# Kernel optimization log

Hardware: AMD Instinct MI355X
Metric: run time of the kernel (lower is better)

Reference implementation:

```python
import jax, jax.numpy as jnp
import numpy as np

TAU = 0.07
EPS = 1e-12  # torch F.normalize eps


def _conv2d(x, w, b, stride):
    # x: (N, Cin, H, W), w: (Cout, Cin, kh, kw)
    y = jax.lax.conv_general_dilated(
        x, w, window_strides=(stride, stride), padding='SAME',
        dimension_numbers=('NCHW', 'OIHW', 'NCHW'))
    return y + b[None, :, None, None]


def _encoder(x, conv1_w, conv1_b, conv2_w, conv2_b, lin_w, lin_b):
    # x: (BTN, 1, H, W) -> (BTN, emb_dim)
    h = jax.nn.relu(_conv2d(x, conv1_w, conv1_b, 2))   # (BTN, 32, H/2, W/2)
    h = jax.nn.relu(_conv2d(h, conv2_w, conv2_b, 2))   # (BTN, 64, H/4, W/4)
    h = h.mean(axis=(2, 3))                            # global avg pool -> (BTN, 64)
    return h @ lin_w + lin_b                           # (BTN, emb_dim)


def setup_inputs() -> dict:
    key = jax.random.key(0)
    ks = jax.random.split(key, 4)
    B, T, N, H, W = 8, 10, 128, 32, 32
    seq = jax.random.normal(ks[0], (B, T, N, H, W), dtype=jnp.float32)
    conv1_w = jax.random.normal(ks[1], (32, 1, 3, 3), dtype=jnp.float32) * (1.0 / 3.0)
    conv1_b = jnp.zeros((32,), jnp.float32)
    conv2_w = jax.random.normal(ks[2], (64, 32, 3, 3), dtype=jnp.float32) * (1.0 / np.sqrt(32 * 9))
    conv2_b = jnp.zeros((64,), jnp.float32)
    lin_w = jax.random.normal(ks[3], (64, 128), dtype=jnp.float32) * (1.0 / 8.0)
    lin_b = jnp.zeros((128,), jnp.float32)
    return {"seq": seq, "conv1_w": conv1_w, "conv1_b": conv1_b,
            "conv2_w": conv2_w, "conv2_b": conv2_b, "lin_w": lin_w, "lin_b": lin_b}


def reference(seq, conv1_w, conv1_b, conv2_w, conv2_b, lin_w, lin_b):
    B, T, N, H, W = seq.shape
    x = seq.reshape(-1, 1, H, W)
    emb = _encoder(x, conv1_w, conv1_b, conv2_w, conv2_b, lin_w, lin_b)
    emb = emb.reshape(B, T, N, -1)
    # L2 normalize along feature dim (torch F.normalize semantics)
    nrm = jnp.sqrt(jnp.sum(emb * emb, axis=-1, keepdims=True))
    emb = emb / jnp.maximum(nrm, EPS)
    # pairwise affinities between consecutive frames: (B, T-1, N, N)
    A = jnp.einsum('btnc,btmc->btnm', emb[:, :-1], emb[:, 1:]) / TAU
    # forward + time-reversed (transposed) affinities: (B, 2(T-1), N, N)
    AA = jnp.concatenate([A, jnp.swapaxes(jnp.flip(A, axis=1), -1, -2)], axis=1)
    S = jax.nn.softmax(AA, axis=-1)  # row-stochastic transition matrices
    I = jnp.eye(N, dtype=seq.dtype)
    loss = jnp.zeros((), seq.dtype)
    for k in range(1, T - 1):
        S_this = jnp.concatenate([S[:, :k], S[:, -k:]], axis=1)  # (B, 2k, N, N)
        At = jnp.broadcast_to(I, (B, N, N))
        for t in range(1, 2 * k):  # note: index 0 unused, matching original
            At = jnp.matmul(S_this[:, t], At)
        # cross_entropy(input=At (B,C=N,d=N), target=eye) with soft targets:
        # mean over (B, d) of -log_softmax(At, class_dim=1)[b, j, j]
        logp = jax.nn.log_softmax(At, axis=1)
        loss = loss - jnp.mean(jnp.diagonal(logp, axis1=1, axis2=2))
    return (loss / N, A)
```

## Files before the change

kernel.cpp:

```cpp
#include <hip/hip_runtime.h>
#include <math.h>

typedef _Float16 f16;
typedef f16 f16x8 __attribute__((ext_vector_type(8)));
typedef f16 f16x4 __attribute__((ext_vector_type(4)));
typedef float f32x4 __attribute__((ext_vector_type(4)));

__global__ __launch_bounds__(256) void k_repack(const float* __restrict__ w2,
                                                const float* __restrict__ w1,
                                                const float* __restrict__ lw,
                                                f16* __restrict__ w2p,
                                                f16* __restrict__ w1p,
                                                float* __restrict__ lwT,
                                                float* __restrict__ lossAcc) {
  const int i = blockIdx.x * 256 + threadIdx.x;
  if (i == 0) lossAcc[0] = 0.f;
  if (i < 18432) {
    const int ic = i & 31, oc = (i >> 5) & 63, tap = i >> 11;
    const float w = w2[oc * 288 + ic * 9 + tap];
    const f16 wh = (f16)w;
    w2p[i] = wh;
    w2p[18432 + i] = (f16)(w - (float)wh);
  }
  if (i < 1024) {
    const int oc = i >> 5, k = i & 31;
    f16 r = (f16)0.f;
    if (k < 9) r = (f16)w1[oc * 9 + k];
    else if (k >= 16 && k < 25) {
      const float w = w1[oc * 9 + (k - 16)];
      r = (f16)(w - (float)((f16)w));
    }
    w1p[i] = r;
  }
  if (i < 8192) lwT[i] = lw[(i & 63) * 128 + (i >> 6)];
}

__global__ __launch_bounds__(256, 4) void k_encoder(
    const float* __restrict__ seq,
    const f16* __restrict__ w1p, const float* __restrict__ b1,
    const f16* __restrict__ w2p, const float* __restrict__ b2,
    const float* __restrict__ lwT, const float* __restrict__ lb,
    f16* __restrict__ emb16)
{
  __shared__ float s_in[33 * 33];
  __shared__ __align__(16) f16 s_h1[289 * 40];
  __shared__ __align__(16) float s_pool[64];
  __shared__ float s_part[2];
  const int t = threadIdx.x, lane = t & 63, wv = t >> 6;
  const int lr = lane & 15, lg = lane >> 4;

  const float* x = seq + (size_t)blockIdx.x * 1024;
  for (int i = t; i < 1024; i += 256)
    s_in[(i >> 5) * 33 + (i & 31)] = x[i];
  if (t < 33) s_in[32 * 33 + t] = 0.f;
  if (t < 32) s_in[t * 33 + 32] = 0.f;
  if (t < 132) {
    const int zi = t >> 2, ch = t & 3;
    const int row = (zi < 16) ? zi * 17 + 16 : 272 + (zi - 16);
    *(f32x4*)&s_h1[row * 40 + ch * 8] = f32x4{0.f, 0.f, 0.f, 0.f};
  }
  f16x8 w1f[2];
  float b1v[2];
#pragma unroll
  for (int n = 0; n < 2; ++n) {
    w1f[n] = *(const f16x8*)(w1p + (n * 16 + lr) * 32 + lg * 8);
    b1v[n] = b1[n * 16 + lr];
  }
  __syncthreads();

  {
    const bool odd = lg & 1;
    f32x4 a1[4][2];
#pragma unroll
    for (int m = 0; m < 4; ++m) {
      const int oy = wv * 4 + m;
      const int base = 66 * oy + 2 * lr;
      f16x8 af;
      af[0] = (f16)s_in[base + (odd ? 68 : 0)];
      { const float v = s_in[base + 1];  af[1] = odd ? (f16)0.f : (f16)v; }
      { const float v = s_in[base + 2];  af[2] = odd ? (f16)0.f : (f16)v; }
      { const float v = s_in[base + 33]; af[3] = odd ? (f16)0.f : (f16)v; }
      { const float v = s_in[base + 34]; af[4] = odd ? (f16)0.f : (f16)v; }
      { const float v = s_in[base + 35]; af[5] = odd ? (f16)0.f : (f16)v; }
      { const float v = s_in[base + 66]; af[6] = odd ? (f16)0.f : (f16)v; }
      { const float v = s_in[base + 67]; af[7] = odd ? (f16)0.f : (f16)v; }
#pragma unroll
      for (int n = 0; n < 2; ++n) {
        const f32x4 c0 = f32x4{b1v[n], b1v[n], b1v[n], b1v[n]};
        a1[m][n] = __builtin_amdgcn_mfma_f32_16x16x32_f16(af, w1f[n], c0, 0, 0, 0);
      }
    }
#pragma unroll
    for (int m = 0; m < 4; ++m) {
      const int oy = wv * 4 + m;
#pragma unroll
      for (int n = 0; n < 2; ++n)
#pragma unroll
        for (int v = 0; v < 4; ++v)
          s_h1[(oy * 17 + lg * 4 + v) * 40 + n * 16 + lr] = (f16)fmaxf(a1[m][n][v], 0.f);
    }
  }
  f16x8 bh[9], bl[9];
  float bias2;
  {
    const int oc = wv * 16 + lr;
#pragma unroll
    for (int tap = 0; tap < 9; ++tap) {
      bh[tap] = *(const f16x8*)(w2p + ((tap * 64 + oc) * 32 + lg * 8));
      bl[tap] = *(const f16x8*)(w2p + 18432 + ((tap * 64 + oc) * 32 + lg * 8));
    }
    bias2 = b2[oc];
  }
  __syncthreads();

  {
    f32x4 acc[4];
#pragma unroll
    for (int m = 0; m < 4; ++m) acc[m] = f32x4{bias2, bias2, bias2, bias2};
#pragma unroll
    for (int m = 0; m < 4; ++m) {
      const int opos = m * 16 + lr, oy = opos >> 3, ox = opos & 7;
      const int baddr = (34 * oy + 2 * ox) * 40 + lg * 8;
#pragma unroll
      for (int dy = 0; dy < 3; ++dy)
#pragma unroll
        for (int dx = 0; dx < 3; ++dx) {
          const int tap = dy * 3 + dx;
          const f16x8 afr = *(const f16x8*)&s_h1[baddr + (dy * 17 + dx) * 40];
          acc[m] = __builtin_amdgcn_mfma_f32_16x16x32_f16(afr, bh[tap], acc[m], 0, 0, 0);
          acc[m] = __builtin_amdgcn_mfma_f32_16x16x32_f16(afr, bl[tap], acc[m], 0, 0, 0);
        }
    }
    float s = 0.f;
#pragma unroll
    for (int m = 0; m < 4; ++m)
#pragma unroll
      for (int v = 0; v < 4; ++v) s += fmaxf(acc[m][v], 0.f);
    s += __shfl_xor(s, 16, 64);
    s += __shfl_xor(s, 32, 64);
    if (lane < 16) s_pool[wv * 16 + lane] = s * (1.f / 64.f);
  }
  __syncthreads();
  float val = 0.f;
  if (t < 128) {
    val = lb[t];
    const float* lrow = lwT + t * 64;
#pragma unroll
    for (int c4 = 0; c4 < 16; ++c4) {
      const f32x4 wv4 = *(const f32x4*)(lrow + c4 * 4);
      const f32x4 pv = *(const f32x4*)&s_pool[c4 * 4];
      val = fmaf(pv[0], wv4[0], val);
      val = fmaf(pv[1], wv4[1], val);
      val = fmaf(pv[2], wv4[2], val);
      val = fmaf(pv[3], wv4[3], val);
    }
  }
  float sq = val * val;
#pragma unroll
  for (int off = 1; off < 64; off <<= 1) sq += __shfl_xor(sq, off, 64);
  if (t < 128 && (t & 63) == 0) s_part[t >> 6] = sq;
  __syncthreads();
  if (t < 128) {
    const float nrm = sqrtf(s_part[0] + s_part[1]);
    emb16[(size_t)blockIdx.x * 128 + t] = (f16)(val / fmaxf(nrm, 1e-12f));
  }
}

__global__ __launch_bounds__(256) void k_affsm(
    const f16* __restrict__ emb16, float* __restrict__ Aout,
    f16* __restrict__ Srow, f16* __restrict__ ST, float* __restrict__ loss)
{
  __shared__ __align__(16) f16 sL[16384];
  __shared__ __align__(16) f16 sR[16384];
  __shared__ __align__(16) f16 sT[128 * 136];
  __shared__ float s_cm[128], s_cd[128];
  __shared__ float s_red4[512];
  __shared__ float s_lred[4];
  const int bid = blockIdx.x, b = bid / 9, tt = bid % 9;
  const int t = threadIdx.x, lane = t & 63, w = t >> 6;
  const int lr = lane & 15, lg = lane >> 4;
  const f16* Ea = emb16 + (size_t)(b * 10 + tt) * 16384;
  const f16* Eb = Ea + 16384;
#pragma unroll
  for (int j = 0; j < 8; ++j) {
    const int ck = j * 256 + t, row = ck >> 4, c16 = ck & 15;
    const int off = ((row << 8) + (c16 << 4)) ^ ((row & 7) << 4);
    *(f16x8*)((char*)sL + off) = *(const f16x8*)(Ea + ck * 8);
    *(f16x8*)((char*)sR + off) = *(const f16x8*)(Eb + ck * 8);
  }
  __syncthreads();
  f32x4 acc[2][8] = {};
#pragma unroll
  for (int kt = 0; kt < 4; ++kt) {
    int row = w * 32 + lr;
    int byt = ((row << 8) + kt * 64 + (lg << 4)) ^ ((row & 7) << 4);
    const f16x8 a0 = *(const f16x8*)((char*)sL + byt);
    row += 16;
    byt = ((row << 8) + kt * 64 + (lg << 4)) ^ ((row & 7) << 4);
    const f16x8 a1 = *(const f16x8*)((char*)sL + byt);
#pragma unroll
    for (int nt = 0; nt < 8; ++nt) {
      const int rb = nt * 16 + lr;
      const int bb = ((rb << 8) + kt * 64 + (lg << 4)) ^ ((rb & 7) << 4);
      const f16x8 bv = *(const f16x8*)((char*)sR + bb);
      acc[0][nt] = __builtin_amdgcn_mfma_f32_16x16x32_f16(a0, bv, acc[0][nt], 0, 0, 0);
      acc[1][nt] = __builtin_amdgcn_mfma_f32_16x16x32_f16(a1, bv, acc[1][nt], 0, 0, 0);
    }
  }
#pragma unroll
  for (int mt = 0; mt < 2; ++mt)
#pragma unroll
    for (int nt = 0; nt < 8; ++nt)
#pragma unroll
      for (int v = 0; v < 4; ++v) acc[mt][nt][v] *= (1.f / 0.07f);

  float* Og = Aout + (size_t)bid * 16384;
#pragma unroll
  for (int mt = 0; mt < 2; ++mt)
#pragma unroll
    for (int nt = 0; nt < 8; ++nt)
#pragma unroll
      for (int v = 0; v < 4; ++v)
        Og[(w * 32 + mt * 16 + lg * 4 + v) * 128 + nt * 16 + lr] = acc[mt][nt][v];

  float rm[2][4], rd[2][4];
#pragma unroll
  for (int mt = 0; mt < 2; ++mt)
#pragma unroll
    for (int v = 0; v < 4; ++v) {
      float m = -1e30f;
#pragma unroll
      for (int nt = 0; nt < 8; ++nt) m = fmaxf(m, acc[mt][nt][v]);
      m = fmaxf(m, __shfl_xor(m, 1, 64));
      m = fmaxf(m, __shfl_xor(m, 2, 64));
      m = fmaxf(m, __shfl_xor(m, 4, 64));
      m = fmaxf(m, __shfl_xor(m, 8, 64));
      float s = 0.f;
#pragma unroll
      for (int nt = 0; nt < 8; ++nt) s += expf(acc[mt][nt][v] - m);
      s += __shfl_xor(s, 1, 64);
      s += __shfl_xor(s, 2, 64);
      s += __shfl_xor(s, 4, 64);
      s += __shfl_xor(s, 8, 64);
      rm[mt][v] = m;
      rd[mt][v] = 1.f / s;
    }
#pragma unroll
  for (int nt = 0; nt < 8; ++nt) {
    float m = -1e30f;
#pragma unroll
    for (int mt = 0; mt < 2; ++mt)
#pragma unroll
      for (int v = 0; v < 4; ++v) m = fmaxf(m, acc[mt][nt][v]);
    m = fmaxf(m, __shfl_xor(m, 16, 64));
    m = fmaxf(m, __shfl_xor(m, 32, 64));
    if (lg == 0) s_red4[(nt * 16 + lr) * 4 + w] = m;
  }
  __syncthreads();
  if (t < 128) s_cm[t] = fmaxf(fmaxf(s_red4[t * 4], s_red4[t * 4 + 1]),
                               fmaxf(s_red4[t * 4 + 2], s_red4[t * 4 + 3]));
  __syncthreads();
#pragma unroll
  for (int nt = 0; nt < 8; ++nt) {
    const float mc = s_cm[nt * 16 + lr];
    float s = 0.f;
#pragma unroll
    for (int mt = 0; mt < 2; ++mt)
#pragma unroll
      for (int v = 0; v < 4; ++v) s += expf(acc[mt][nt][v] - mc);
    s += __shfl_xor(s, 16, 64);
    s += __shfl_xor(s, 32, 64);
    if (lg == 0) s_red4[(nt * 16 + lr) * 4 + w] = s;
  }
  __syncthreads();
  if (t < 128) s_cd[t] = 1.f / (s_red4[t * 4] + s_red4[t * 4 + 1] +
                                s_red4[t * 4 + 2] + s_red4[t * 4 + 3]);
  __syncthreads();

  const bool wantSfD = (tt >= 2 && tt <= 7);
  const bool wantSfT = (tt == 1);
  const bool wantSbD = (tt >= 1 && tt <= 7);
  const bool wantSbT = (tt == 0);
  f16* SfD = Srow + (size_t)(b * 18 + tt) * 16384;
  f16* SbD = ST + (size_t)(b * 18 + 17 - tt) * 16384;

  float contrib = 0.f;
#pragma unroll
  for (int mt = 0; mt < 2; ++mt)
#pragma unroll
    for (int v = 0; v < 4; ++v) {
      const int r = w * 32 + mt * 16 + lg * 4 + v;
      float qsum = 0.f, dval = 0.f;
#pragma unroll
      for (int nt = 0; nt < 8; ++nt) {
        const int c = nt * 16 + lr;
        const float a = acc[mt][nt][v];
        const float sf = expf(a - rm[mt][v]) * rd[mt][v];
        const float sb = expf(a - s_cm[c]) * s_cd[c];
        if (wantSfD) SfD[r * 128 + c] = (f16)sf;
        if (wantSbD) SbD[r * 128 + c] = (f16)sb;
        if (wantSfT) sT[c * 136 + r] = (f16)sf;
        if (wantSbT) {
          sT[c * 136 + r] = (f16)sb;
          qsum += expf(sb);
          if (nt == (w * 2 + mt)) dval = sb;
        }
      }
      if (wantSbT) {
        qsum += __shfl_xor(qsum, 1, 64);
        qsum += __shfl_xor(qsum, 2, 64);
        qsum += __shfl_xor(qsum, 4, 64);
        qsum += __shfl_xor(qsum, 8, 64);
        if (lr == lg * 4 + v) contrib += dval - logf(qsum);
      }
    }
  if (wantSfT || wantSbT) {
    __syncthreads();
    f16* dst = wantSfT ? (ST + (size_t)(b * 18 + 1) * 16384)
                       : (Srow + (size_t)(b * 18 + 17) * 16384);
#pragma unroll
    for (int j = 0; j < 8; ++j) {
      const int e = (j * 256 + t) * 8;
      *(f16x8*)(dst + e) = *(const f16x8*)&sT[(e >> 7) * 136 + (e & 127)];
    }
  }
  if (wantSbT) {
#pragma unroll
    for (int off = 1; off < 64; off <<= 1) contrib += __shfl_xor(contrib, off, 64);
    if (lane == 0) s_lred[w] = contrib;
    __syncthreads();
    if (t == 0) atomicAdd(loss, s_lred[0] + s_lred[1] + s_lred[2] + s_lred[3]);
  }
}

__global__ __launch_bounds__(256) void k_chain(
    int k,
    const f16* __restrict__ Srow, const f16* __restrict__ ST,
    f16* __restrict__ Pcur, const f16* __restrict__ Pprev,
    f16* __restrict__ FTcur, const f16* __restrict__ FTprev,
    float* __restrict__ loss)
{
  __shared__ __align__(16) f16 sL[16384];
  __shared__ __align__(16) f16 sRt[16384];
  const int role = blockIdx.x >> 3, b = blockIdx.x & 7;
  const int t = threadIdx.x, lane = t & 63, w = t >> 6;
  const int lr = lane & 15, lg = lane >> 4;

  const f16 *L, *Rt;
  if (role == 0) {
    if (k > 8) return;
    L = (k == 2) ? (Srow + (size_t)(b * 18 + 17) * 16384) : (Pprev + (size_t)b * 16384);
    Rt = ST + (size_t)(b * 18 + (18 - k)) * 16384;
  } else if (role == 1) {
    if (k < 3 || k > 8) return;
    L = Srow + (size_t)(b * 18 + (k - 1)) * 16384;
    Rt = (k == 3) ? (ST + (size_t)(b * 18 + 1) * 16384) : (FTprev + (size_t)b * 16384);
  } else {
    if (k < 3) return;
    L = Pprev + (size_t)b * 16384;
    Rt = (k == 3) ? (ST + (size_t)(b * 18 + 1) * 16384) : (FTprev + (size_t)b * 16384);
  }
#pragma unroll
  for (int j = 0; j < 8; ++j) {
    const int ck = j * 256 + t, row = ck >> 4, c16 = ck & 15;
    const int off = ((row << 8) + (c16 << 4)) ^ ((row & 7) << 4);
    *(f16x8*)((char*)sL + off) = *(const f16x8*)(L + ck * 8);
    *(f16x8*)((char*)sRt + off) = *(const f16x8*)(Rt + ck * 8);
  }
  __syncthreads();
  f32x4 acc[2][8] = {};
#pragma unroll
  for (int kt = 0; kt < 4; ++kt) {
    int row = w * 32 + lr;
    int byt = ((row << 8) + kt * 64 + (lg << 4)) ^ ((row & 7) << 4);
    const f16x8 a0 = *(const f16x8*)((char*)sL + byt);
    row += 16;
    byt = ((row << 8) + kt * 64 + (lg << 4)) ^ ((row & 7) << 4);
    const f16x8 a1 = *(const f16x8*)((char*)sL + byt);
#pragma unroll
    for (int nt = 0; nt < 8; ++nt) {
      const int rb = nt * 16 + lr;
      const int bb = ((rb << 8) + kt * 64 + (lg << 4)) ^ ((rb & 7) << 4);
      const f16x8 bv = *(const f16x8*)((char*)sRt + bb);
      acc[0][nt] = __builtin_amdgcn_mfma_f32_16x16x32_f16(a0, bv, acc[0][nt], 0, 0, 0);
      acc[1][nt] = __builtin_amdgcn_mfma_f32_16x16x32_f16(a1, bv, acc[1][nt], 0, 0, 0);
    }
  }
  if (role == 0) {
    f16* P = Pcur + (size_t)b * 16384;
#pragma unroll
    for (int mt = 0; mt < 2; ++mt)
#pragma unroll
      for (int nt = 0; nt < 8; ++nt)
#pragma unroll
        for (int v = 0; v < 4; ++v)
          P[(w * 32 + mt * 16 + lg * 4 + v) * 128 + nt * 16 + lr] = (f16)acc[mt][nt][v];
  } else if (role == 1) {
    f16* FT = FTcur + (size_t)b * 16384;
#pragma unroll
    for (int mt = 0; mt < 2; ++mt)
#pragma unroll
      for (int nt = 0; nt < 8; ++nt) {
        f16x4 pk;
#pragma unroll
        for (int v = 0; v < 4; ++v) pk[v] = (f16)acc[mt][nt][v];
        *(f16x4*)(FT + (size_t)(nt * 16 + lr) * 128 + w * 32 + mt * 16 + lg * 4) = pk;
      }
  } else {
    __syncthreads();
    float* redm = (float*)sL;
    float* redM = redm + 512;
    float* reds = redM + 128;
    float* redL = reds + 512;
    float* redW = redL + 128;
#pragma unroll
    for (int nt = 0; nt < 8; ++nt) {
      float pm = -1e30f;
#pragma unroll
      for (int mt = 0; mt < 2; ++mt)
#pragma unroll
        for (int v = 0; v < 4; ++v) pm = fmaxf(pm, acc[mt][nt][v]);
      pm = fmaxf(pm, __shfl_xor(pm, 16, 64));
      pm = fmaxf(pm, __shfl_xor(pm, 32, 64));
      if (lg == 0) redm[(nt * 16 + lr) * 4 + w] = pm;
    }
    __syncthreads();
    if (t < 128) redM[t] = fmaxf(fmaxf(redm[t * 4], redm[t * 4 + 1]),
                                 fmaxf(redm[t * 4 + 2], redm[t * 4 + 3]));
    __syncthreads();
#pragma unroll
    for (int nt = 0; nt < 8; ++nt) {
      const float mc = redM[nt * 16 + lr];
      float ps = 0.f;
#pragma unroll
      for (int mt = 0; mt < 2; ++mt)
#pragma unroll
        for (int v = 0; v < 4; ++v) ps += expf(acc[mt][nt][v] - mc);
      ps += __shfl_xor(ps, 16, 64);
      ps += __shfl_xor(ps, 32, 64);
      if (lg == 0) reds[(nt * 16 + lr) * 4 + w] = ps;
    }
    __syncthreads();
    if (t < 128) redL[t] = logf(reds[t * 4] + reds[t * 4 + 1] +
                                reds[t * 4 + 2] + reds[t * 4 + 3]);
    __syncthreads();
    float contrib = 0.f;
#pragma unroll
    for (int mt = 0; mt < 2; ++mt)
#pragma unroll
      for (int nt = 0; nt < 8; ++nt)
#pragma unroll
        for (int v = 0; v < 4; ++v) {
          const int r = w * 32 + mt * 16 + lg * 4 + v, c = nt * 16 + lr;
          if (r == c) contrib += acc[mt][nt][v] - redM[c] - redL[c];
        }
#pragma unroll
    for (int off = 1; off < 64; off <<= 1) contrib += __shfl_xor(contrib, off, 64);
    if (lane == 0) redW[w] = contrib;
    __syncthreads();
    if (t == 0) atomicAdd(loss, redW[0] + redW[1] + redW[2] + redW[3]);
  }
}

__global__ void k_final(const float* __restrict__ acc, float* __restrict__ out) {
  out[0] = -acc[0] * (1.f / 131072.f);
}

extern "C" void kernel_launch(void* const* d_in, const int* in_sizes, int n_in,
                              void* d_out, int out_size, void* d_ws, size_t ws_size,
                              hipStream_t stream) {
  const float* seq = (const float*)d_in[0];
  const float* w1  = (const float*)d_in[1];
  const float* b1  = (const float*)d_in[2];
  const float* w2  = (const float*)d_in[3];
  const float* b2  = (const float*)d_in[4];
  const float* lw  = (const float*)d_in[5];
  const float* lb  = (const float*)d_in[6];
  float* out = (float*)d_out;

  f16* emb16 = (f16*)d_ws;
  f16* Srow  = emb16 + 1310720;
  f16* ST    = Srow + 2359296;
  f16* Pb    = ST + 2359296;
  f16* FTb   = Pb + 262144;
  f16* w2p   = FTb + 262144;
  f16* w1p   = w2p + 36864;
  float* lwT = (float*)(w1p + 1024);
  float* lossAcc = lwT + 8192;

  float* Aout = out + 1;

  k_repack<<<72, 256, 0, stream>>>(w2, w1, lw, w2p, w1p, lwT, lossAcc);
  k_encoder<<<10240, 256, 0, stream>>>(seq, w1p, b1, w2p, b2, lwT, lb, emb16);
  k_affsm<<<72, 256, 0, stream>>>(emb16, Aout, Srow, ST, lossAcc);
  for (int k = 2; k <= 9; ++k) {
    const int cur = k & 1, prev = cur ^ 1;
    k_chain<<<24, 256, 0, stream>>>(k, Srow, ST,
        Pb + cur * 131072, Pb + prev * 131072,
        FTb + cur * 131072, FTb + prev * 131072,
        lossAcc);
  }
  k_final<<<1, 1, 0, stream>>>(lossAcc, out);
}
```

Measured before the change: 276.5 us.

## Replace sequential chain matmuls with parallel prefix scan and retune encoder LDS

The eight dependent k_chain launches (24 blocks each) are replaced by a three-step Hillis-Steele prefix scan over the transition matrices in both directions (128 blocks per step), followed by one parallel loss kernel. The goal is to cut the serial dependency depth and the launch count, and to fill more CUs. To support this, k_affsm now writes both row and transposed forms of every softmax matrix. The encoder separately stores its input tile in fp16 with tighter LDS padding and raises the occupancy hint from 4 to 6. In exchange the scan does more total matmuls and more global traffic, and its fp16 intermediates round differently.

```diff
diff --git a/kernel.cpp b/kernel.cpp
--- a/kernel.cpp
+++ b/kernel.cpp
@@ -2,9 +2,43 @@
 #include <math.h>
 
 typedef _Float16 f16;
+typedef f16 f16x2 __attribute__((ext_vector_type(2)));
+typedef f16 f16x4 __attribute__((ext_vector_type(4)));
 typedef f16 f16x8 __attribute__((ext_vector_type(8)));
-typedef f16 f16x4 __attribute__((ext_vector_type(4)));
 typedef float f32x4 __attribute__((ext_vector_type(4)));
+
+__device__ __forceinline__ void stage_pair(const f16* __restrict__ L,
+                                           const f16* __restrict__ Rt,
+                                           f16* sL, f16* sRt, int t) {
+#pragma unroll
+  for (int j = 0; j < 8; ++j) {
+    const int ck = j * 256 + t, row = ck >> 4, c16 = ck & 15;
+    const int off = ((row << 8) + (c16 << 4)) ^ ((row & 7) << 4);
+    *(f16x8*)((char*)sL + off) = *(const f16x8*)(L + ck * 8);
+    *(f16x8*)((char*)sRt + off) = *(const f16x8*)(Rt + ck * 8);
+  }
+}
+
+__device__ __forceinline__ void mm128(const f16* sL, const f16* sRt,
+                                      f32x4 acc[2][8], int w, int lr, int lg) {
+#pragma unroll
+  for (int kt = 0; kt < 4; ++kt) {
+    int row = w * 32 + lr;
+    int byt = ((row << 8) + kt * 64 + (lg << 4)) ^ ((row & 7) << 4);
+    const f16x8 a0 = *(const f16x8*)((const char*)sL + byt);
+    row += 16;
+    byt = ((row << 8) + kt * 64 + (lg << 4)) ^ ((row & 7) << 4);
+    const f16x8 a1 = *(const f16x8*)((const char*)sL + byt);
+#pragma unroll
+    for (int nt = 0; nt < 8; ++nt) {
+      const int rb = nt * 16 + lr;
+      const int bb = ((rb << 8) + kt * 64 + (lg << 4)) ^ ((rb & 7) << 4);
+      const f16x8 bv = *(const f16x8*)((const char*)sRt + bb);
+      acc[0][nt] = __builtin_amdgcn_mfma_f32_16x16x32_f16(a0, bv, acc[0][nt], 0, 0, 0);
+      acc[1][nt] = __builtin_amdgcn_mfma_f32_16x16x32_f16(a1, bv, acc[1][nt], 0, 0, 0);
+    }
+  }
+}
 
 __global__ __launch_bounds__(256) void k_repack(const float* __restrict__ w2,
                                                 const float* __restrict__ w1,
@@ -35,29 +69,33 @@
   if (i < 8192) lwT[i] = lw[(i & 63) * 128 + (i >> 6)];
 }
 
-__global__ __launch_bounds__(256, 4) void k_encoder(
+__global__ __launch_bounds__(256, 6) void k_encoder(
     const float* __restrict__ seq,
     const f16* __restrict__ w1p, const float* __restrict__ b1,
     const f16* __restrict__ w2p, const float* __restrict__ b2,
     const float* __restrict__ lwT, const float* __restrict__ lb,
     f16* __restrict__ emb16)
 {
-  __shared__ float s_in[33 * 33];
-  __shared__ __align__(16) f16 s_h1[289 * 40];
+  __shared__ __align__(16) f16 s_in16[33 * 34];
+  __shared__ __align__(16) f16 s_h1[289 * 36];
   __shared__ __align__(16) float s_pool[64];
   __shared__ float s_part[2];
   const int t = threadIdx.x, lane = t & 63, wv = t >> 6;
   const int lr = lane & 15, lg = lane >> 4;
 
-  const float* x = seq + (size_t)blockIdx.x * 1024;
-  for (int i = t; i < 1024; i += 256)
-    s_in[(i >> 5) * 33 + (i & 31)] = x[i];
-  if (t < 33) s_in[32 * 33 + t] = 0.f;
-  if (t < 32) s_in[t * 33 + 32] = 0.f;
-  if (t < 132) {
-    const int zi = t >> 2, ch = t & 3;
-    const int row = (zi < 16) ? zi * 17 + 16 : 272 + (zi - 16);
-    *(f32x4*)&s_h1[row * 40 + ch * 8] = f32x4{0.f, 0.f, 0.f, 0.f};
+  {
+    const float* x = seq + (size_t)blockIdx.x * 1024;
+    const f32x4 v4 = *(const f32x4*)(x + t * 4);
+    const int row = t >> 3, col = (t & 7) * 4;
+    *(f16x2*)&s_in16[row * 34 + col] = f16x2{(f16)v4[0], (f16)v4[1]};
+    *(f16x2*)&s_in16[row * 34 + col + 2] = f16x2{(f16)v4[2], (f16)v4[3]};
+  }
+  if (t < 32) { s_in16[t * 34 + 32] = (f16)0.f; s_in16[t * 34 + 33] = (f16)0.f; }
+  if (t < 34) s_in16[32 * 34 + t] = (f16)0.f;
+  for (int zi = t; zi < 264; zi += 256) {
+    const int rr = zi >> 3, ch = zi & 7;
+    const int row = (rr < 16) ? rr * 17 + 16 : 272 + (rr - 16);
+    *(f16x4*)&s_h1[row * 36 + ch * 4] = f16x4{(f16)0.f, (f16)0.f, (f16)0.f, (f16)0.f};
   }
   f16x8 w1f[2];
   float b1v[2];
@@ -74,16 +112,16 @@
 #pragma unroll
     for (int m = 0; m < 4; ++m) {
       const int oy = wv * 4 + m;
-      const int base = 66 * oy + 2 * lr;
+      const int base = 68 * oy + 2 * lr;
       f16x8 af;
-      af[0] = (f16)s_in[base + (odd ? 68 : 0)];
-      { const float v = s_in[base + 1];  af[1] = odd ? (f16)0.f : (f16)v; }
-      { const float v = s_in[base + 2];  af[2] = odd ? (f16)0.f : (f16)v; }
-      { const float v = s_in[base + 33]; af[3] = odd ? (f16)0.f : (f16)v; }
-      { const float v = s_in[base + 34]; af[4] = odd ? (f16)0.f : (f16)v; }
-      { const float v = s_in[base + 35]; af[5] = odd ? (f16)0.f : (f16)v; }
-      { const float v = s_in[base + 66]; af[6] = odd ? (f16)0.f : (f16)v; }
-      { const float v = s_in[base + 67]; af[7] = odd ? (f16)0.f : (f16)v; }
+      if (odd) {
+        af = f16x8{s_in16[base + 70], (f16)0.f, (f16)0.f, (f16)0.f,
+                   (f16)0.f, (f16)0.f, (f16)0.f, (f16)0.f};
+      } else {
+        af[0] = s_in16[base];      af[1] = s_in16[base + 1];  af[2] = s_in16[base + 2];
+        af[3] = s_in16[base + 34]; af[4] = s_in16[base + 35]; af[5] = s_in16[base + 36];
+        af[6] = s_in16[base + 68]; af[7] = s_in16[base + 69];
+      }
 #pragma unroll
       for (int n = 0; n < 2; ++n) {
         const f32x4 c0 = f32x4{b1v[n], b1v[n], b1v[n], b1v[n]};
@@ -97,7 +135,7 @@
       for (int n = 0; n < 2; ++n)
 #pragma unroll
         for (int v = 0; v < 4; ++v)
-          s_h1[(oy * 17 + lg * 4 + v) * 40 + n * 16 + lr] = (f16)fmaxf(a1[m][n][v], 0.f);
+          s_h1[(oy * 17 + lg * 4 + v) * 36 + n * 16 + lr] = (f16)fmaxf(a1[m][n][v], 0.f);
     }
   }
   f16x8 bh[9], bl[9];
@@ -120,13 +158,13 @@
 #pragma unroll
     for (int m = 0; m < 4; ++m) {
       const int opos = m * 16 + lr, oy = opos >> 3, ox = opos & 7;
-      const int baddr = (34 * oy + 2 * ox) * 40 + lg * 8;
+      const int baddr = (34 * oy + 2 * ox) * 36 + lg * 8;
 #pragma unroll
       for (int dy = 0; dy < 3; ++dy)
 #pragma unroll
         for (int dx = 0; dx < 3; ++dx) {
           const int tap = dy * 3 + dx;
-          const f16x8 afr = *(const f16x8*)&s_h1[baddr + (dy * 17 + dx) * 40];
+          const f16x8 afr = *(const f16x8*)&s_h1[baddr + (dy * 17 + dx) * 36];
           acc[m] = __builtin_amdgcn_mfma_f32_16x16x32_f16(afr, bh[tap], acc[m], 0, 0, 0);
           acc[m] = __builtin_amdgcn_mfma_f32_16x16x32_f16(afr, bl[tap], acc[m], 0, 0, 0);
         }
@@ -180,33 +218,10 @@
   const int t = threadIdx.x, lane = t & 63, w = t >> 6;
   const int lr = lane & 15, lg = lane >> 4;
   const f16* Ea = emb16 + (size_t)(b * 10 + tt) * 16384;
-  const f16* Eb = Ea + 16384;
-#pragma unroll
-  for (int j = 0; j < 8; ++j) {
-    const int ck = j * 256 + t, row = ck >> 4, c16 = ck & 15;
-    const int off = ((row << 8) + (c16 << 4)) ^ ((row & 7) << 4);
-    *(f16x8*)((char*)sL + off) = *(const f16x8*)(Ea + ck * 8);
-    *(f16x8*)((char*)sR + off) = *(const f16x8*)(Eb + ck * 8);
-  }
+  stage_pair(Ea, Ea + 16384, sL, sR, t);
   __syncthreads();
   f32x4 acc[2][8] = {};
-#pragma unroll
-  for (int kt = 0; kt < 4; ++kt) {
-    int row = w * 32 + lr;
-    int byt = ((row << 8) + kt * 64 + (lg << 4)) ^ ((row & 7) << 4);
-    const f16x8 a0 = *(const f16x8*)((char*)sL + byt);
-    row += 16;
-    byt = ((row << 8) + kt * 64 + (lg << 4)) ^ ((row & 7) << 4);
-    const f16x8 a1 = *(const f16x8*)((char*)sL + byt);
-#pragma unroll
-    for (int nt = 0; nt < 8; ++nt) {
-      const int rb = nt * 16 + lr;
-      const int bb = ((rb << 8) + kt * 64 + (lg << 4)) ^ ((rb & 7) << 4);
-      const f16x8 bv = *(const f16x8*)((char*)sR + bb);
-      acc[0][nt] = __builtin_amdgcn_mfma_f32_16x16x32_f16(a0, bv, acc[0][nt], 0, 0, 0);
-      acc[1][nt] = __builtin_amdgcn_mfma_f32_16x16x32_f16(a1, bv, acc[1][nt], 0, 0, 0);
-    }
-  }
+  mm128(sL, sR, acc, w, lr, lg);
 #pragma unroll
   for (int mt = 0; mt < 2; ++mt)
 #pragma unroll
@@ -222,6 +237,8 @@
 #pragma unroll
       for (int v = 0; v < 4; ++v)
         Og[(w * 32 + mt * 16 + lg * 4 + v) * 128 + nt * 16 + lr] = acc[mt][nt][v];
+
+  if (tt == 8) return;
 
   float rm[2][4], rd[2][4];
 #pragma unroll
@@ -277,12 +294,10 @@
                                 s_red4[t * 4 + 2] + s_red4[t * 4 + 3]);
   __syncthreads();
 
-  const bool wantSfD = (tt >= 2 && tt <= 7);
-  const bool wantSfT = (tt == 1);
-  const bool wantSbD = (tt >= 1 && tt <= 7);
-  const bool wantSbT = (tt == 0);
-  f16* SfD = Srow + (size_t)(b * 18 + tt) * 16384;
-  f16* SbD = ST + (size_t)(b * 18 + 17 - tt) * 16384;
+  f16* SfRow = Srow + (size_t)(b * 18 + tt) * 16384;
+  f16* SfT   = ST   + (size_t)(b * 18 + tt) * 16384;
+  f16* SbT   = ST   + (size_t)(b * 18 + 17 - tt) * 16384;
+  f16* SbRow = Srow + (size_t)(b * 18 + 17 - tt) * 16384;
 
   float contrib = 0.f;
 #pragma unroll
@@ -297,16 +312,15 @@
         const float a = acc[mt][nt][v];
         const float sf = expf(a - rm[mt][v]) * rd[mt][v];
         const float sb = expf(a - s_cm[c]) * s_cd[c];
-        if (wantSfD) SfD[r * 128 + c] = (f16)sf;
-        if (wantSbD) SbD[r * 128 + c] = (f16)sb;
-        if (wantSfT) sT[c * 136 + r] = (f16)sf;
-        if (wantSbT) {
-          sT[c * 136 + r] = (f16)sb;
+        SfRow[r * 128 + c] = (f16)sf;
+        SbT[r * 128 + c] = (f16)sb;
+        sT[c * 136 + r] = (f16)sf;
+        if (tt == 0) {
           qsum += expf(sb);
           if (nt == (w * 2 + mt)) dval = sb;
         }
       }
-      if (wantSbT) {
+      if (tt == 0) {
         qsum += __shfl_xor(qsum, 1, 64);
         qsum += __shfl_xor(qsum, 2, 64);
         qsum += __shfl_xor(qsum, 4, 64);
@@ -314,17 +328,34 @@
         if (lr == lg * 4 + v) contrib += dval - logf(qsum);
       }
     }
-  if (wantSfT || wantSbT) {
-    __syncthreads();
-    f16* dst = wantSfT ? (ST + (size_t)(b * 18 + 1) * 16384)
-                       : (Srow + (size_t)(b * 18 + 17) * 16384);
+  __syncthreads();
+  if (tt >= 1) {
 #pragma unroll
     for (int j = 0; j < 8; ++j) {
       const int e = (j * 256 + t) * 8;
-      *(f16x8*)(dst + e) = *(const f16x8*)&sT[(e >> 7) * 136 + (e & 127)];
-    }
-  }
-  if (wantSbT) {
+      *(f16x8*)(SfT + e) = *(const f16x8*)&sT[(e >> 7) * 136 + (e & 127)];
+    }
+  }
+  __syncthreads();
+#pragma unroll
+  for (int mt = 0; mt < 2; ++mt)
+#pragma unroll
+    for (int v = 0; v < 4; ++v) {
+      const int r = w * 32 + mt * 16 + lg * 4 + v;
+#pragma unroll
+      for (int nt = 0; nt < 8; ++nt) {
+        const int c = nt * 16 + lr;
+        const float sb = expf(acc[mt][nt][v] - s_cm[c]) * s_cd[c];
+        sT[c * 136 + r] = (f16)sb;
+      }
+    }
+  __syncthreads();
+#pragma unroll
+  for (int j = 0; j < 8; ++j) {
+    const int e = (j * 256 + t) * 8;
+    *(f16x8*)(SbRow + e) = *(const f16x8*)&sT[(e >> 7) * 136 + (e & 127)];
+  }
+  if (tt == 0) {
 #pragma unroll
     for (int off = 1; off < 64; off <<= 1) contrib += __shfl_xor(contrib, off, 64);
     if (lane == 0) s_lred[w] = contrib;
@@ -333,133 +364,145 @@
   }
 }
 
-__global__ __launch_bounds__(256) void k_chain(
-    int k,
+__global__ __launch_bounds__(256) void k_scan(
+    const int step,
     const f16* __restrict__ Srow, const f16* __restrict__ ST,
-    f16* __restrict__ Pcur, const f16* __restrict__ Pprev,
-    f16* __restrict__ FTcur, const f16* __restrict__ FTprev,
+    f16* __restrict__ scanR, f16* __restrict__ scanT)
+{
+  __shared__ __align__(16) f16 sL[16384];
+  __shared__ __align__(16) f16 sRt[16384];
+  const int bid = blockIdx.x;
+  const int dir = bid >> 6, b = bid & 7, i = ((bid >> 3) & 7) + 1;
+  if (dir == 1 && i == 8) return;
+  const int s = 1 << step;
+  const int inpp = (step == 2) ? 1 : 0;
+  const int outpp = (step == 1) ? 1 : 0;
+  const int t = threadIdx.x, lane = t & 63, w = t >> 6;
+  const int lr = lane & 15, lg = lane >> 4;
+
+#define SLOT_R(pp, d, ii) (scanR + ((((size_t)(pp) * 2 + (d)) * 9 + (ii)) * 8 + b) * 16384)
+#define SLOT_T(pp, d, ii) (scanT + ((((size_t)(pp) * 2 + (d)) * 9 + (ii)) * 8 + b) * 16384)
+
+  f16* outR = SLOT_R(outpp, dir, i);
+  f16* outT = SLOT_T(outpp, dir, i);
+
+  if (i <= s) {
+    const f16 *srcR, *srcT;
+    if (step == 0) {
+      const int j = (dir == 0) ? (18 - i) : i;
+      srcR = Srow + (size_t)(b * 18 + j) * 16384;
+      srcT = ST + (size_t)(b * 18 + j) * 16384;
+    } else {
+      srcR = SLOT_R(inpp, dir, i);
+      srcT = SLOT_T(inpp, dir, i);
+    }
+    for (int j = t; j < 2048; j += 256) {
+      *(f16x8*)(outR + j * 8) = *(const f16x8*)(srcR + j * 8);
+      *(f16x8*)(outT + j * 8) = *(const f16x8*)(srcT + j * 8);
+    }
+    return;
+  }
+  const f16 *L, *Rt;
+  if (step == 0) {
+    if (dir == 0) { L = Srow + (size_t)(b * 18 + (19 - i)) * 16384;
+                    Rt = ST + (size_t)(b * 18 + (18 - i)) * 16384; }
+    else          { L = Srow + (size_t)(b * 18 + i) * 16384;
+                    Rt = ST + (size_t)(b * 18 + (i - 1)) * 16384; }
+  } else {
+    if (dir == 0) { L = SLOT_R(inpp, 0, i - s); Rt = SLOT_T(inpp, 0, i); }
+    else          { L = SLOT_R(inpp, 1, i);     Rt = SLOT_T(inpp, 1, i - s); }
+  }
+  stage_pair(L, Rt, sL, sRt, t);
+  __syncthreads();
+  f32x4 acc[2][8] = {};
+  mm128(sL, sRt, acc, w, lr, lg);
+#pragma unroll
+  for (int mt = 0; mt < 2; ++mt)
+#pragma unroll
+    for (int nt = 0; nt < 8; ++nt)
+#pragma unroll
+      for (int v = 0; v < 4; ++v)
+        outR[(w * 32 + mt * 16 + lg * 4 + v) * 128 + nt * 16 + lr] = (f16)acc[mt][nt][v];
+#pragma unroll
+  for (int mt = 0; mt < 2; ++mt)
+#pragma unroll
+    for (int nt = 0; nt < 8; ++nt) {
+      f16x4 pk;
+#pragma unroll
+      for (int v = 0; v < 4; ++v) pk[v] = (f16)acc[mt][nt][v];
+      *(f16x4*)(outT + (size_t)(nt * 16 + lr) * 128 + w * 32 + mt * 16 + lg * 4) = pk;
+    }
+#undef SLOT_R
+#undef SLOT_T
+}
+
+__global__ __launch_bounds__(256) void k_loss(
+    const f16* __restrict__ scanR, const f16* __restrict__ scanT,
     float* __restrict__ loss)
 {
   __shared__ __align__(16) f16 sL[16384];
   __shared__ __align__(16) f16 sRt[16384];
-  const int role = blockIdx.x >> 3, b = blockIdx.x & 7;
+  const int b = blockIdx.x & 7, k = (blockIdx.x >> 3) + 2;
   const int t = threadIdx.x, lane = t & 63, w = t >> 6;
   const int lr = lane & 15, lg = lane >> 4;
-
-  const f16 *L, *Rt;
-  if (role == 0) {
-    if (k > 8) return;
-    L = (k == 2) ? (Srow + (size_t)(b * 18 + 17) * 16384) : (Pprev + (size_t)b * 16384);
-    Rt = ST + (size_t)(b * 18 + (18 - k)) * 16384;
-  } else if (role == 1) {
-    if (k < 3 || k > 8) return;
-    L = Srow + (size_t)(b * 18 + (k - 1)) * 16384;
-    Rt = (k == 3) ? (ST + (size_t)(b * 18 + 1) * 16384) : (FTprev + (size_t)b * 16384);
-  } else {
-    if (k < 3) return;
-    L = Pprev + (size_t)b * 16384;
-    Rt = (k == 3) ? (ST + (size_t)(b * 18 + 1) * 16384) : (FTprev + (size_t)b * 16384);
-  }
-#pragma unroll
-  for (int j = 0; j < 8; ++j) {
-    const int ck = j * 256 + t, row = ck >> 4, c16 = ck & 15;
-    const int off = ((row << 8) + (c16 << 4)) ^ ((row & 7) << 4);
-    *(f16x8*)((char*)sL + off) = *(const f16x8*)(L + ck * 8);
-    *(f16x8*)((char*)sRt + off) = *(const f16x8*)(Rt + ck * 8);
-  }
+  const f16* L = scanR + (((size_t)0 * 9 + k) * 8 + b) * 16384;
+  const f16* Rt = scanT + ((((size_t)0 * 2 + 1) * 9 + (k - 1)) * 8 + b) * 16384;
+  stage_pair(L, Rt, sL, sRt, t);
   __syncthreads();
   f32x4 acc[2][8] = {};
-#pragma unroll
-  for (int kt = 0; kt < 4; ++kt) {
-    int row = w * 32 + lr;
-    int byt = ((row << 8) + kt * 64 + (lg << 4)) ^ ((row & 7) << 4);
-    const f16x8 a0 = *(const f16x8*)((char*)sL + byt);
-    row += 16;
-    byt = ((row << 8) + kt * 64 + (lg << 4)) ^ ((row & 7) << 4);
-    const f16x8 a1 = *(const f16x8*)((char*)sL + byt);
-#pragma unroll
-    for (int nt = 0; nt < 8; ++nt) {
-      const int rb = nt * 16 + lr;
-      const int bb = ((rb << 8) + kt * 64 + (lg << 4)) ^ ((rb & 7) << 4);
-      const f16x8 bv = *(const f16x8*)((char*)sRt + bb);
-      acc[0][nt] = __builtin_amdgcn_mfma_f32_16x16x32_f16(a0, bv, acc[0][nt], 0, 0, 0);
-      acc[1][nt] = __builtin_amdgcn_mfma_f32_16x16x32_f16(a1, bv, acc[1][nt], 0, 0, 0);
-    }
-  }
-  if (role == 0) {
-    f16* P = Pcur + (size_t)b * 16384;
+  mm128(sL, sRt, acc, w, lr, lg);
+  __syncthreads();
+  float* redm = (float*)sL;
+  float* redM = redm + 512;
+  float* reds = redM + 128;
+  float* redL = reds + 512;
+  float* redW = redL + 128;
+#pragma unroll
+  for (int nt = 0; nt < 8; ++nt) {
+    float pm = -1e30f;
 #pragma unroll
     for (int mt = 0; mt < 2; ++mt)
 #pragma unroll
-      for (int nt = 0; nt < 8; ++nt)
-#pragma unroll
-        for (int v = 0; v < 4; ++v)
-          P[(w * 32 + mt * 16 + lg * 4 + v) * 128 + nt * 16 + lr] = (f16)acc[mt][nt][v];
-  } else if (role == 1) {
-    f16* FT = FTcur + (size_t)b * 16384;
+      for (int v = 0; v < 4; ++v) pm = fmaxf(pm, acc[mt][nt][v]);
+    pm = fmaxf(pm, __shfl_xor(pm, 16, 64));
+    pm = fmaxf(pm, __shfl_xor(pm, 32, 64));
+    if (lg == 0) redm[(nt * 16 + lr) * 4 + w] = pm;
+  }
+  __syncthreads();
+  if (t < 128) redM[t] = fmaxf(fmaxf(redm[t * 4], redm[t * 4 + 1]),
+                               fmaxf(redm[t * 4 + 2], redm[t * 4 + 3]));
+  __syncthreads();
+#pragma unroll
+  for (int nt = 0; nt < 8; ++nt) {
+    const float mc = redM[nt * 16 + lr];
+    float ps = 0.f;
 #pragma unroll
     for (int mt = 0; mt < 2; ++mt)
 #pragma unroll
-      for (int nt = 0; nt < 8; ++nt) {
-        f16x4 pk;
-#pragma unroll
-        for (int v = 0; v < 4; ++v) pk[v] = (f16)acc[mt][nt][v];
-        *(f16x4*)(FT + (size_t)(nt * 16 + lr) * 128 + w * 32 + mt * 16 + lg * 4) = pk;
+      for (int v = 0; v < 4; ++v) ps += expf(acc[mt][nt][v] - mc);
+    ps += __shfl_xor(ps, 16, 64);
+    ps += __shfl_xor(ps, 32, 64);
+    if (lg == 0) reds[(nt * 16 + lr) * 4 + w] = ps;
+  }
+  __syncthreads();
+  if (t < 128) redL[t] = logf(reds[t * 4] + reds[t * 4 + 1] +
+                              reds[t * 4 + 2] + reds[t * 4 + 3]);
+  __syncthreads();
+  float contrib = 0.f;
+#pragma unroll
+  for (int mt = 0; mt < 2; ++mt)
+#pragma unroll
+    for (int nt = 0; nt < 8; ++nt)
+#pragma unroll
+      for (int v = 0; v < 4; ++v) {
+        const int r = w * 32 + mt * 16 + lg * 4 + v, c = nt * 16 + lr;
+        if (r == c) contrib += acc[mt][nt][v] - redM[c] - redL[c];
       }
-  } else {
-    __syncthreads();
-    float* redm = (float*)sL;
-    float* redM = redm + 512;
-    float* reds = redM + 128;
-    float* redL = reds + 512;
-    float* redW = redL + 128;
-#pragma unroll
-    for (int nt = 0; nt < 8; ++nt) {
-      float pm = -1e30f;
-#pragma unroll
-      for (int mt = 0; mt < 2; ++mt)
-#pragma unroll
-        for (int v = 0; v < 4; ++v) pm = fmaxf(pm, acc[mt][nt][v]);
-      pm = fmaxf(pm, __shfl_xor(pm, 16, 64));
-      pm = fmaxf(pm, __shfl_xor(pm, 32, 64));
-      if (lg == 0) redm[(nt * 16 + lr) * 4 + w] = pm;
-    }
-    __syncthreads();
-    if (t < 128) redM[t] = fmaxf(fmaxf(redm[t * 4], redm[t * 4 + 1]),
-                                 fmaxf(redm[t * 4 + 2], redm[t * 4 + 3]));
-    __syncthreads();
-#pragma unroll
-    for (int nt = 0; nt < 8; ++nt) {
-      const float mc = redM[nt * 16 + lr];
-      float ps = 0.f;
-#pragma unroll
-      for (int mt = 0; mt < 2; ++mt)
-#pragma unroll
-        for (int v = 0; v < 4; ++v) ps += expf(acc[mt][nt][v] - mc);
-      ps += __shfl_xor(ps, 16, 64);
-      ps += __shfl_xor(ps, 32, 64);
-      if (lg == 0) reds[(nt * 16 + lr) * 4 + w] = ps;
-    }
-    __syncthreads();
-    if (t < 128) redL[t] = logf(reds[t * 4] + reds[t * 4 + 1] +
-                                reds[t * 4 + 2] + reds[t * 4 + 3]);
-    __syncthreads();
-    float contrib = 0.f;
-#pragma unroll
-    for (int mt = 0; mt < 2; ++mt)
-#pragma unroll
-      for (int nt = 0; nt < 8; ++nt)
-#pragma unroll
-        for (int v = 0; v < 4; ++v) {
-          const int r = w * 32 + mt * 16 + lg * 4 + v, c = nt * 16 + lr;
-          if (r == c) contrib += acc[mt][nt][v] - redM[c] - redL[c];
-        }
-#pragma unroll
-    for (int off = 1; off < 64; off <<= 1) contrib += __shfl_xor(contrib, off, 64);
-    if (lane == 0) redW[w] = contrib;
-    __syncthreads();
-    if (t == 0) atomicAdd(loss, redW[0] + redW[1] + redW[2] + redW[3]);
-  }
+#pragma unroll
+  for (int off = 1; off < 64; off <<= 1) contrib += __shfl_xor(contrib, off, 64);
+  if (lane == 0) redW[w] = contrib;
+  __syncthreads();
+  if (t == 0) atomicAdd(loss, redW[0] + redW[1] + redW[2] + redW[3]);
 }
 
 __global__ void k_final(const float* __restrict__ acc, float* __restrict__ out) {
@@ -481,9 +524,9 @@
   f16* emb16 = (f16*)d_ws;
   f16* Srow  = emb16 + 1310720;
   f16* ST    = Srow + 2359296;
-  f16* Pb    = ST + 2359296;
-  f16* FTb   = Pb + 262144;
-  f16* w2p   = FTb + 262144;
+  f16* scanR = ST + 2359296;
+  f16* scanT = scanR + 4718592;
+  f16* w2p   = scanT + 4718592;
   f16* w1p   = w2p + 36864;
   float* lwT = (float*)(w1p + 1024);
   float* lossAcc = lwT + 8192;
@@ -493,12 +536,9 @@
   k_repack<<<72, 256, 0, stream>>>(w2, w1, lw, w2p, w1p, lwT, lossAcc);
   k_encoder<<<10240, 256, 0, stream>>>(seq, w1p, b1, w2p, b2, lwT, lb, emb16);
   k_affsm<<<72, 256, 0, stream>>>(emb16, Aout, Srow, ST, lossAcc);
-  for (int k = 2; k <= 9; ++k) {
-    const int cur = k & 1, prev = cur ^ 1;
-    k_chain<<<24, 256, 0, stream>>>(k, Srow, ST,
-        Pb + cur * 131072, Pb + prev * 131072,
-        FTb + cur * 131072, FTb + prev * 131072,
-        lossAcc);
-  }
+  k_scan<<<128, 256, 0, stream>>>(0, Srow, ST, scanR, scanT);
+  k_scan<<<128, 256, 0, stream>>>(1, Srow, ST, scanR, scanT);
+  k_scan<<<128, 256, 0, stream>>>(2, Srow, ST, scanR, scanT);
+  k_loss<<<56, 256, 0, stream>>>(scanR, scanT, lossAcc);
   k_final<<<1, 1, 0, stream>>>(lossAcc, out);
 }
```

Result: slower. 419.4 us (+51.7%).
